# Kernel optimization log

Hardware: AMD Instinct MI355X
Metric: run time of the kernel (lower is better)

Reference implementation:

```python
import math
import jax, jax.numpy as jnp
import numpy as np

EPS = 1e-5

def lstm(x, Wih, Whh, b):
    # x: [N,T,D]; PyTorch gate order i,f,g,o; b = b_ih + b_hh combined
    N = x.shape[0]
    H = Whh.shape[1]
    gx = jnp.einsum('ntd,gd->ntg', x, Wih) + b  # [N,T,4H]
    def step(carry, g):
        h, c = carry
        z = g + h @ Whh.T
        i, f, gg, o = jnp.split(z, 4, axis=-1)
        c = jax.nn.sigmoid(f) * c + jax.nn.sigmoid(i) * jnp.tanh(gg)
        h = jax.nn.sigmoid(o) * jnp.tanh(c)
        return (h, c), h
    init = (jnp.zeros((N, H), x.dtype), jnp.zeros((N, H), x.dtype))
    (hN, _), ys = jax.lax.scan(step, init, jnp.swapaxes(gx, 0, 1))
    return jnp.swapaxes(ys, 0, 1), hN  # outputs [N,T,H], h_n [N,H]

def bilstm_layer(x, fW, fU, fb, bW, bU, bb):
    of, _ = lstm(x, fW, fU, fb)
    ob, _ = lstm(x[:, ::-1], bW, bU, bb)
    return jnp.concatenate([of, ob[:, ::-1]], axis=-1)

def layernorm(x, g, b):
    m = jnp.mean(x, -1, keepdims=True)
    v = jnp.mean((x - m) ** 2, -1, keepdims=True)
    return (x - m) * jax.lax.rsqrt(v + EPS) * g + b

def encoder_layer(src, Wq, bq, Wk, bk, Wv, bv, Wo, bo, W1, b1, W2, b2, lng, lnb):
    B, S, d = src.shape
    G, NH = 5, 5
    dk = d // NH
    # group channel shuffle (as in source)
    qs = src.reshape(B, S, G, d // G).swapaxes(-1, -2).reshape(B, S, d)
    q = qs @ Wq.T + bq
    k = q @ Wk.T + bk   # NOTE: source applies W_k/W_v to the projected query
    v = q @ Wv.T + bv
    def heads(t):
        return t.reshape(B, S, NH, dk).transpose(0, 2, 1, 3)
    qh, kh, vh = heads(q), heads(k), heads(v)
    attn = jax.nn.softmax(jnp.einsum('bhqd,bhkd->bhqk', qh, kh) / math.sqrt(dk), axis=-1)
    o = jnp.einsum('bhqk,bhkd->bhqd', attn, vh).transpose(0, 2, 1, 3).reshape(B, S, d)
    o = o @ Wo.T + bo
    src = layernorm(src + o, lng, lnb)          # dropout is identity in eval
    ff = jax.nn.relu(src @ W1.T + b1) @ W2.T + b2
    src = layernorm(src + ff, lng, lnb)         # same LayerNorm params reused
    return src, attn

def _forward(x, qWih, qWhh, qb, kWih, kWhh, kb, vWih, vWhh, vb,
             tWq, tbq, tWk, tbk, tWv, tbv, tWo, tbo, tW1, tb1, tW2, tb2, tlng, tlnb,
             l0fWih, l0fWhh, l0fb, l0bWih, l0bWhh, l0bb,
             l1fWih, l1fWhh, l1fb, l1bWih, l1bWhh, l1bb,
             fc1W, fc1b, fc2W, fc2b):
    B, T, F = x.shape
    H = qWhh.shape[1]
    # per-feature LSTMs: shared weights across features -> batch them
    xf = x.transpose(0, 2, 1).reshape(B * F, T, 1)
    _, hq = lstm(xf, qWih, qWhh, qb)   # [B*F,H]
    _, hk = lstm(xf, kWih, kWhh, kb)   # [B*F,H]
    _, hv = lstm(xf, vWih, vWhh, vb)   # [B*F,1]
    Q = hq.reshape(B, F, H)
    K = hk.reshape(B, F, H)
    V = hv.reshape(B, F)
    # b_ij = (q_i . k_j)/sqrt(H) * v_j, softmax over j
    scores = jnp.einsum('bih,bjh->bij', Q, K) / math.sqrt(H) * V[:, None, :]
    Wsm = jax.nn.softmax(scores, axis=-1)          # [B,F,F] rows indexed by i
    attn_output = jnp.einsum('btj,bij->bti', x, Wsm)  # bmm(x, softmax_b_i)
    b = Wsm.transpose(0, 2, 1)                     # stack(b_list, dim=-1)
    src = jnp.concatenate([x, attn_output], axis=-1)  # [B,T,2F]
    attns = []
    for l in range(2):
        src, a = encoder_layer(src, tWq[l], tbq[l], tWk[l], tbk[l], tWv[l], tbv[l],
                               tWo[l], tbo[l], tW1[l], tb1[l], tW2[l], tb2[l],
                               tlng[l], tlnb[l])
        attns.append(a)
    c = jnp.stack(attns)                           # [2,B,5,T,T]
    out = bilstm_layer(src, l0fWih, l0fWhh, l0fb, l0bWih, l0bWhh, l0bb)
    out = bilstm_layer(out, l1fWih, l1fWhh, l1fb, l1bWih, l1bWhh, l1bb)
    out = jax.nn.relu(out[:, -1, :])               # [B,2H]
    out = jax.nn.relu(out @ fc1W.T + fc1b)
    out = out @ fc2W.T + fc2b                      # [B,1]
    return out, b, c

def setup_inputs() -> dict:
    B, T, F, H = 16, 128, 40, 64
    d = 2 * F
    key = jax.random.key(0)
    ks = iter(jax.random.split(key, 64))
    def n(shape, fan):
        return (jax.random.normal(next(ks), shape) / math.sqrt(fan)).astype(jnp.float32)
    inp = {'x': jax.random.normal(next(ks), (B, T, F), dtype=jnp.float32)}
    # per-feature LSTMs
    inp.update(qWih=n((4 * H, 1), 1), qWhh=n((4 * H, H), H), qb=n((4 * H,), H))
    inp.update(kWih=n((4 * H, 1), 1), kWhh=n((4 * H, H), H), kb=n((4 * H,), H))
    inp.update(vWih=n((4, 1), 1), vWhh=n((4, 1), 1), vb=n((4,), 1))
    # transformer (2 layers stacked on leading axis)
    inp.update(tWq=n((2, d, d), d), tbq=n((2, d), d), tWk=n((2, d, d), d), tbk=n((2, d), d),
               tWv=n((2, d, d), d), tbv=n((2, d), d), tWo=n((2, d, d), d), tbo=n((2, d), d),
               tW1=n((2, 4 * d, d), d), tb1=n((2, 4 * d), d), tW2=n((2, d, 4 * d), 4 * d),
               tb2=n((2, d), 4 * d), tlng=jnp.ones((2, d), jnp.float32), tlnb=jnp.zeros((2, d), jnp.float32))
    # main bidirectional 2-layer LSTM
    inp.update(l0fWih=n((4 * H, d), d), l0fWhh=n((4 * H, H), H), l0fb=n((4 * H,), H),
               l0bWih=n((4 * H, d), d), l0bWhh=n((4 * H, H), H), l0bb=n((4 * H,), H),
               l1fWih=n((4 * H, 2 * H), 2 * H), l1fWhh=n((4 * H, H), H), l1fb=n((4 * H,), H),
               l1bWih=n((4 * H, 2 * H), 2 * H), l1bWhh=n((4 * H, H), H), l1bb=n((4 * H,), H))
    inp.update(fc1W=n((H, 2 * H), 2 * H), fc1b=n((H,), 2 * H), fc2W=n((1, H), H), fc2b=n((1,), H))
    return inp

def reference(x, qWih, qWhh, qb, kWih, kWhh, kb, vWih, vWhh, vb,
              tWq, tbq, tWk, tbk, tWv, tbv, tWo, tbo, tW1, tb1, tW2, tb2, tlng, tlnb,
              l0fWih, l0fWhh, l0fb, l0bWih, l0bWhh, l0bb,
              l1fWih, l1fWhh, l1fb, l1bWih, l1bWhh, l1bb,
              fc1W, fc1b, fc2W, fc2b):
    return _forward(x, qWih, qWhh, qb, kWih, kWhh, kb, vWih, vWhh, vb,
                    tWq, tbq, tWk, tbk, tWv, tbv, tWo, tbo, tW1, tb1, tW2, tb2, tlng, tlnb,
                    l0fWih, l0fWhh, l0fb, l0bWih, l0bWhh, l0bb,
                    l1fWih, l1fWhh, l1fb, l1bWih, l1bWhh, l1bb,
                    fc1W, fc1b, fc2W, fc2b)
```

## Files before the change

### kernel.cpp

```cpp
#include <hip/hip_runtime.h>

__device__ __forceinline__ float sigf(float x){ return 1.0f/(1.0f+__expf(-x)); }
__device__ __forceinline__ float tanhfast(float x){ return 1.0f - 2.0f/(__expf(2.0f*x)+1.0f); }

#define Bn 16
#define Tn 128
#define Fn 40
#define Hn 64
#define Dn 80
#define NHn 5
#define DKn 16
#define FFn 320

#define LD4(p,i) (((const float4*)(p))[i])

#define DECL16(v, p) \
  float4 v##0=LD4(p,0),  v##1=LD4(p,1),  v##2=LD4(p,2),  v##3=LD4(p,3),  \
         v##4=LD4(p,4),  v##5=LD4(p,5),  v##6=LD4(p,6),  v##7=LD4(p,7),  \
         v##8=LD4(p,8),  v##9=LD4(p,9),  v##10=LD4(p,10),v##11=LD4(p,11),\
         v##12=LD4(p,12),v##13=LD4(p,13),v##14=LD4(p,14),v##15=LD4(p,15);
#define PIN4(P) asm volatile("" : "+v"(P.x), "+v"(P.y), "+v"(P.z), "+v"(P.w));
#define PIN16(v) PIN4(v##0) PIN4(v##1) PIN4(v##2) PIN4(v##3) PIN4(v##4) PIN4(v##5) \
  PIN4(v##6) PIN4(v##7) PIN4(v##8) PIN4(v##9) PIN4(v##10) PIN4(v##11) PIN4(v##12) \
  PIN4(v##13) PIN4(v##14) PIN4(v##15)

#define ACC1(i) { const float4 hv = hb4[i]; \
  a += hv.x*w##i.x + hv.y*w##i.y + hv.z*w##i.z + hv.w*w##i.w; }
#define ACCROW ACC1(0) ACC1(1) ACC1(2) ACC1(3) ACC1(4) ACC1(5) ACC1(6) ACC1(7) \
  ACC1(8) ACC1(9) ACC1(10) ACC1(11) ACC1(12) ACC1(13) ACC1(14) ACC1(15)

__global__ __launch_bounds__(256) __attribute__((amdgpu_waves_per_eu(1,4)))
void k_feat_lstm4(
    const float* __restrict__ x,
    const float* __restrict__ qWih, const float* __restrict__ qWhh, const float* __restrict__ qb,
    const float* __restrict__ kWih, const float* __restrict__ kWhh, const float* __restrict__ kb,
    const float* __restrict__ vWih, const float* __restrict__ vWhh, const float* __restrict__ vb,
    float* __restrict__ hq, float* __restrict__ hk, float* __restrict__ hv)
{
  const int blk = blockIdx.x;
  const int t = threadIdx.x;
  if (blk >= 1280){
    const int inst = (blk - 1280)*256 + t;
    if (inst < 640){
      const int bi = inst/Fn, f = inst%Fn;
      const float* xp = x + bi*Tn*Fn + f;
      const float wih0=vWih[0], wih1=vWih[1], wih2=vWih[2], wih3=vWih[3];
      const float u0v=vWhh[0], u1v=vWhh[1], u2v=vWhh[2], u3v=vWhh[3];
      const float c0=vb[0], c1=vb[1], c2=vb[2], c3=vb[3];
      float h=0.f, c=0.f;
      #pragma unroll 1
      for (int tt=0;tt<Tn;++tt){
        float xt = xp[tt*Fn];
        float zi = xt*wih0 + h*u0v + c0;
        float zf = xt*wih1 + h*u1v + c1;
        float zg = xt*wih2 + h*u2v + c2;
        float zo = xt*wih3 + h*u3v + c3;
        c = sigf(zf)*c + sigf(zi)*tanhfast(zg);
        h = sigf(zo)*tanhfast(c);
      }
      hv[inst] = h;
    }
    return;
  }
  const bool isk = blk >= 640;
  const int inst = isk ? blk-640 : blk;
  const int bi = inst/Fn, f = inst%Fn;
  const float* Whh = isk ? kWhh : qWhh;
  const float* Wih = isk ? kWih : qWih;
  const float* bia = isk ? kb  : qb;
  float* outp = isk ? hk : hq;

  DECL16(w, Whh + t*Hn);
  PIN16(w);
  const float wih = Wih[t];
  const float bb  = bia[t];

  __shared__ __align__(16) float hb[Hn];
  __shared__ float zb[4*Hn];
  __shared__ float xls[Tn];

  const float* xp = x + bi*Tn*Fn + f;
  if (t < Tn) xls[t] = xp[t*Fn];
  if (t < Hn) hb[t] = 0.f;
  float c = 0.f, h = 0.f;
  __syncthreads();

  const float4* hb4 = (const float4*)hb;
  #pragma unroll 1
  for (int tt=0;tt<Tn;++tt){
    const float xt = xls[tt];
    float a = bb + xt*wih;
    ACCROW
    zb[t] = a;
    __syncthreads();
    if (t < Hn){
      const float zi = zb[t], zf = zb[t+64], zg = zb[t+128], zo = zb[t+192];
      c = sigf(zf)*c + sigf(zi)*tanhfast(zg);
      h = sigf(zo)*tanhfast(c);
      hb[t] = h;
    }
    __syncthreads();
  }
  if (t < Hn) outp[inst*Hn + t] = h;
}

__global__ __launch_bounds__(64) void k_featattn(
    const float* __restrict__ hq, const float* __restrict__ hk, const float* __restrict__ hv,
    float* __restrict__ Wsm, float* __restrict__ out_b)
{
  const int blk = blockIdx.x;
  const int bi = blk / Fn, i = blk % Fn;
  const int j = threadIdx.x;
  __shared__ float qrow[Hn];
  qrow[j] = hq[blk*Hn + j];
  __syncthreads();
  float s = -1e30f;
  if (j < Fn){
    const float* krow = hk + (bi*Fn + j)*Hn;
    float a = 0.f;
    #pragma unroll
    for (int h2=0; h2<Hn; ++h2) a += qrow[h2]*krow[h2];
    s = a * 0.125f * hv[bi*Fn + j];
  }
  float m = s;
  #pragma unroll
  for (int off=32; off>0; off>>=1) m = fmaxf(m, __shfl_xor(m, off));
  float e = (j < Fn) ? __expf(s - m) : 0.f;
  float tot = e;
  #pragma unroll
  for (int off=32; off>0; off>>=1) tot += __shfl_xor(tot, off);
  float p = e / tot;
  if (j < Fn){
    Wsm[blk*Fn + j] = p;
    out_b[bi*(Fn*Fn) + j*Fn + i] = p;
  }
}

__global__ __launch_bounds__(128) void k_build_src(
    const float* __restrict__ x, const float* __restrict__ Wsm, float* __restrict__ src)
{
  const int blk = blockIdx.x;
  const int bi = blk / Tn;
  const int tid = threadIdx.x;
  __shared__ float xrow[Fn];
  if (tid < Fn) xrow[tid] = x[blk*Fn + tid];
  __syncthreads();
  if (tid < Fn){
    src[blk*Dn + tid] = xrow[tid];
  } else if (tid < Dn){
    const int i = tid - Fn;
    const float* wrow = Wsm + (bi*Fn + i)*Fn;
    float a = 0.f;
    #pragma unroll
    for (int j2=0;j2<Fn;++j2) a += xrow[j2]*wrow[j2];
    src[blk*Dn + tid] = a;
  }
}

__global__ __launch_bounds__(128) void k_qkv(
    const float* __restrict__ src,
    const float* __restrict__ Wq, const float* __restrict__ bq,
    const float* __restrict__ Wk, const float* __restrict__ bk,
    const float* __restrict__ Wv, const float* __restrict__ bv,
    float* __restrict__ q, float* __restrict__ k, float* __restrict__ v)
{
  const int row = blockIdx.x;
  const int t = threadIdx.x;
  __shared__ float qs[Dn];
  __shared__ float qrow[Dn];
  if (t < Dn) qs[t] = src[row*Dn + (t%5)*16 + t/5];
  __syncthreads();
  if (t < Dn){
    const float* wr = Wq + t*Dn;
    float a = bq[t];
    #pragma unroll 8
    for (int d2=0; d2<Dn; ++d2) a += qs[d2]*wr[d2];
    qrow[t] = a;
    q[row*Dn + t] = a;
  }
  __syncthreads();
  if (t < Dn){
    const float* wk = Wk + t*Dn;
    const float* wv = Wv + t*Dn;
    float ak = bk[t], av = bv[t];
    #pragma unroll 8
    for (int d2=0; d2<Dn; ++d2){ float qq = qrow[d2]; ak += qq*wk[d2]; av += qq*wv[d2]; }
    k[row*Dn + t] = ak;
    v[row*Dn + t] = av;
  }
}

__global__ __launch_bounds__(128) void k_attn(
    const float* __restrict__ q, const float* __restrict__ k, const float* __restrict__ v,
    float* __restrict__ o, float* __restrict__ c_out)
{
  const int s1 = blockIdx.x, h = blockIdx.y, bi = blockIdx.z;
  const int s2 = threadIdx.x;
  __shared__ float qf[DKn];
  __shared__ float p[Tn];
  __shared__ float red_m[2];
  __shared__ float red_s[2];
  if (s2 < DKn) qf[s2] = q[(bi*Tn + s1)*Dn + h*DKn + s2];
  __syncthreads();
  const float* krow = k + (bi*Tn + s2)*Dn + h*DKn;
  float a = 0.f;
  #pragma unroll
  for (int d2=0; d2<DKn; ++d2) a += qf[d2]*krow[d2];
  a *= 0.25f;
  const int wv_id = s2 >> 6;
  float m = a;
  #pragma unroll
  for (int off=32; off>0; off>>=1) m = fmaxf(m, __shfl_xor(m, off));
  if ((s2 & 63) == 0) red_m[wv_id] = m;
  __syncthreads();
  m = fmaxf(red_m[0], red_m[1]);
  float e = __expf(a - m);
  float tot = e;
  #pragma unroll
  for (int off=32; off>0; off>>=1) tot += __shfl_xor(tot, off);
  if ((s2 & 63) == 0) red_s[wv_id] = tot;
  __syncthreads();
  tot = red_s[0] + red_s[1];
  float pv = e / tot;
  p[s2] = pv;
  c_out[((bi*NHn + h)*Tn + s1)*Tn + s2] = pv;
  __syncthreads();
  if (s2 < DKn){
    const float* vcol = v + bi*Tn*Dn + h*DKn + s2;
    float acc = 0.f;
    for (int j2=0;j2<Tn;++j2) acc += p[j2]*vcol[j2*Dn];
    o[(bi*Tn + s1)*Dn + h*DKn + s2] = acc;
  }
}

__global__ __launch_bounds__(320) void k_oln_ffln(
    const float* __restrict__ o, const float* __restrict__ Wo, const float* __restrict__ bo,
    const float* __restrict__ W1, const float* __restrict__ b1,
    const float* __restrict__ W2, const float* __restrict__ b2,
    const float* __restrict__ lng, const float* __restrict__ lnb, float* __restrict__ src)
{
  const int row = blockIdx.x;
  const int t = threadIdx.x;
  __shared__ float orow[Dn];
  __shared__ float s1row[Dn];
  __shared__ float h1[FFn];
  __shared__ float red[128];
  if (t < Dn) orow[t] = o[row*Dn + t];
  __syncthreads();
  float val = 0.f;
  if (t < Dn){
    const float* wr = Wo + t*Dn;
    float a = bo[t];
    #pragma unroll 8
    for (int d2=0; d2<Dn; ++d2) a += orow[d2]*wr[d2];
    val = a + src[row*Dn + t];
  }
  if (t < 128) red[t] = (t < Dn) ? val : 0.f;
  __syncthreads();
  for (int s=64; s>0; s>>=1){ if (t < s) red[t] += red[t+s]; __syncthreads(); }
  float mean = red[0] * (1.f/Dn);
  __syncthreads();
  if (t < 128){ float dv = (t < Dn) ? (val - mean) : 0.f; red[t] = dv*dv; }
  __syncthreads();
  for (int s=64; s>0; s>>=1){ if (t < s) red[t] += red[t+s]; __syncthreads(); }
  float rstd = rsqrtf(red[0]*(1.f/Dn) + 1e-5f);
  if (t < Dn) s1row[t] = (val - mean)*rstd*lng[t] + lnb[t];
  __syncthreads();
  {
    const float* wr = W1 + t*Dn;
    float a = b1[t];
    #pragma unroll 8
    for (int d2=0; d2<Dn; ++d2) a += s1row[d2]*wr[d2];
    h1[t] = fmaxf(a, 0.f);
  }
  __syncthreads();
  float val2 = 0.f;
  if (t < Dn){
    const float* wr = W2 + t*FFn;
    float a = b2[t];
    #pragma unroll 8
    for (int d2=0; d2<FFn; ++d2) a += h1[d2]*wr[d2];
    val2 = a + s1row[t];
  }
  if (t < 128) red[t] = (t < Dn) ? val2 : 0.f;
  __syncthreads();
  for (int s=64; s>0; s>>=1){ if (t < s) red[t] += red[t+s]; __syncthreads(); }
  mean = red[0] * (1.f/Dn);
  __syncthreads();
  if (t < 128){ float dv = (t < Dn) ? (val2 - mean) : 0.f; red[t] = dv*dv; }
  __syncthreads();
  for (int s=64; s>0; s>>=1){ if (t < s) red[t] += red[t+s]; __syncthreads(); }
  rstd = rsqrtf(red[0]*(1.f/Dn) + 1e-5f);
  if (t < Dn) src[row*Dn + t] = (val2 - mean)*rstd*lng[t] + lnb[t];
}

__global__ __launch_bounds__(256) void k_gx(
    const float* __restrict__ X, int inD,
    const float* __restrict__ WihF, const float* __restrict__ bF,
    const float* __restrict__ WihB, const float* __restrict__ bB,
    float* __restrict__ gx)
{
  const int row = blockIdx.x;
  const int dir = blockIdx.y;
  const int g = threadIdx.x;
  __shared__ float xs[128];
  for (int d2=g; d2<inD; d2+=256) xs[d2] = X[row*inD + d2];
  __syncthreads();
  const float* W  = dir ? WihB : WihF;
  const float* bb = dir ? bB  : bF;
  const float* wr = W + g*inD;
  float a = bb[g];
  for (int d2=0; d2<inD; ++d2) a += xs[d2]*wr[d2];
  gx[dir*(Bn*Tn*256) + row*256 + g] = a;
}

__global__ __launch_bounds__(256) __attribute__((amdgpu_waves_per_eu(1,4)))
void k_bilstm_rec4(
    const float* __restrict__ gx,
    const float* __restrict__ WhhF, const float* __restrict__ WhhB,
    float* __restrict__ outp)
{
  const int n = blockIdx.x;
  const int dir = blockIdx.y;
  const int t = threadIdx.x;
  const float* Whh = dir ? WhhB : WhhF;
  DECL16(w, Whh + t*Hn);
  PIN16(w);

  __shared__ __align__(16) float hb[Hn];
  __shared__ float zb[4*Hn];
  if (t < Hn) hb[t] = 0.f;
  float c = 0.f, h = 0.f;
  __syncthreads();

  const float* gxd = gx + dir*(Bn*Tn*256) + n*Tn*256;
  const float4* hb4 = (const float4*)hb;
  const int t0 = dir ? Tn-1 : 0;
  float g0 = gxd[t0*256 + t];
  #pragma unroll 1
  for (int step=0; step<Tn; ++step){
    const int tt = dir ? (Tn-1-step) : step;
    int tn = dir ? (Tn-2-step) : (step+1);
    tn = max(0, min(Tn-1, tn));
    const float p0 = gxd[tn*256 + t];
    float a = g0;
    ACCROW
    zb[t] = a;
    __syncthreads();
    if (t < Hn){
      const float zi = zb[t], zf = zb[t+64], zg = zb[t+128], zo = zb[t+192];
      c = sigf(zf)*c + sigf(zi)*tanhfast(zg);
      h = sigf(zo)*tanhfast(c);
      hb[t] = h;
      outp[(n*Tn + tt)*128 + dir*Hn + t] = h;
    }
    __syncthreads();
    g0 = p0;
  }
}

__global__ __launch_bounds__(128) void k_final(
    const float* __restrict__ out1,
    const float* __restrict__ fc1W, const float* __restrict__ fc1b,
    const float* __restrict__ fc2W, const float* __restrict__ fc2b,
    float* __restrict__ outp)
{
  const int n = blockIdx.x;
  const int t = threadIdx.x;
  __shared__ float r[128];
  __shared__ float a1[64];
  r[t] = fmaxf(out1[(n*Tn + (Tn-1))*128 + t], 0.f);
  __syncthreads();
  if (t < 64){
    const float* wr = fc1W + t*128;
    float a = fc1b[t];
    #pragma unroll 8
    for (int d2=0; d2<128; ++d2) a += r[d2]*wr[d2];
    a1[t] = fmaxf(a, 0.f);
  }
  __syncthreads();
  if (t == 0){
    float a = fc2b[0];
    #pragma unroll 8
    for (int d2=0; d2<64; ++d2) a += a1[d2]*fc2W[d2];
    outp[n] = a;
  }
}

extern "C" void kernel_launch(void* const* d_in, const int* in_sizes, int n_in,
                              void* d_out, int out_size, void* d_ws, size_t ws_size,
                              hipStream_t stream)
{
  const float* x     = (const float*)d_in[0];
  const float* qWih  = (const float*)d_in[1];
  const float* qWhh  = (const float*)d_in[2];
  const float* qb    = (const float*)d_in[3];
  const float* kWih  = (const float*)d_in[4];
  const float* kWhh  = (const float*)d_in[5];
  const float* kb    = (const float*)d_in[6];
  const float* vWih  = (const float*)d_in[7];
  const float* vWhh  = (const float*)d_in[8];
  const float* vb    = (const float*)d_in[9];
  const float* tWq   = (const float*)d_in[10];
  const float* tbq   = (const float*)d_in[11];
  const float* tWk   = (const float*)d_in[12];
  const float* tbk   = (const float*)d_in[13];
  const float* tWv   = (const float*)d_in[14];
  const float* tbv   = (const float*)d_in[15];
  const float* tWo   = (const float*)d_in[16];
  const float* tbo   = (const float*)d_in[17];
  const float* tW1   = (const float*)d_in[18];
  const float* tb1   = (const float*)d_in[19];
  const float* tW2   = (const float*)d_in[20];
  const float* tb2   = (const float*)d_in[21];
  const float* tlng  = (const float*)d_in[22];
  const float* tlnb  = (const float*)d_in[23];
  const float* l0fWih= (const float*)d_in[24];
  const float* l0fWhh= (const float*)d_in[25];
  const float* l0fb  = (const float*)d_in[26];
  const float* l0bWih= (const float*)d_in[27];
  const float* l0bWhh= (const float*)d_in[28];
  const float* l0bb  = (const float*)d_in[29];
  const float* l1fWih= (const float*)d_in[30];
  const float* l1fWhh= (const float*)d_in[31];
  const float* l1fb  = (const float*)d_in[32];
  const float* l1bWih= (const float*)d_in[33];
  const float* l1bWhh= (const float*)d_in[34];
  const float* l1bb  = (const float*)d_in[35];
  const float* fc1W  = (const float*)d_in[36];
  const float* fc1b  = (const float*)d_in[37];
  const float* fc2W  = (const float*)d_in[38];
  const float* fc2b  = (const float*)d_in[39];

  float* ws  = (float*)d_ws;
  float* hq  = ws;
  float* hk  = hq  + 640*64;
  float* hv  = hk  + 640*64;
  float* Wsm = hv  + 640;
  float* src = Wsm + 16*40*40;
  float* q   = src + 16*128*80;
  float* k   = q   + 16*128*80;
  float* v   = k   + 16*128*80;
  float* o   = v   + 16*128*80;
  float* gx  = o   + 16*128*80;
  float* lout0 = gx + 2*16*128*256;
  float* lout1 = lout0 + 16*128*128;

  float* outp  = (float*)d_out;
  float* out_b = outp + 16;
  float* out_c = out_b + 16*40*40;

  k_feat_lstm4<<<1283, 256, 0, stream>>>(x, qWih,qWhh,qb, kWih,kWhh,kb, vWih,vWhh,vb, hq,hk,hv);
  k_featattn<<<640, 64, 0, stream>>>(hq, hk, hv, Wsm, out_b);
  k_build_src<<<2048, 128, 0, stream>>>(x, Wsm, src);
  for (int l=0; l<2; ++l){
    k_qkv<<<2048, 128, 0, stream>>>(src, tWq + l*Dn*Dn, tbq + l*Dn,
                                    tWk + l*Dn*Dn, tbk + l*Dn,
                                    tWv + l*Dn*Dn, tbv + l*Dn, q, k, v);
    k_attn<<<dim3(128,5,16), 128, 0, stream>>>(q, k, v, o, out_c + (size_t)l*16*5*128*128);
    k_oln_ffln<<<2048, 320, 0, stream>>>(o, tWo + l*Dn*Dn, tbo + l*Dn,
                                         tW1 + l*FFn*Dn, tb1 + l*FFn,
                                         tW2 + l*Dn*FFn, tb2 + l*Dn,
                                         tlng + l*Dn, tlnb + l*Dn, src);
  }
  k_gx<<<dim3(2048,2), 256, 0, stream>>>(src, 80, l0fWih, l0fb, l0bWih, l0bb, gx);
  k_bilstm_rec4<<<dim3(16,2), 256, 0, stream>>>(gx, l0fWhh, l0bWhh, lout0);
  k_gx<<<dim3(2048,2), 256, 0, stream>>>(lout0, 128, l1fWih, l1fb, l1bWih, l1bb, gx);
  k_bilstm_rec4<<<dim3(16,2), 256, 0, stream>>>(gx, l1fWhh, l1bWhh, lout1);
  k_final<<<16, 128, 0, stream>>>(lout1, fc1W, fc1b, fc2W, fc2b, outp);
}
```

Before: 814.5 us.

## Split LSTM recurrent matvec across 4 lanes per gate row with shuffle reduction

The recurrent LSTM kernels (feature LSTMs and the bidirectional main LSTM) now use 1024-thread blocks. Each gate row's 64-wide dot product with h is split across 4 lanes of 16 elements each, and the partial sums are combined with xor shuffles. This shortens the serial per-step matvec latency on the critical recurrent chain and cuts weight registers per thread. The cost is larger blocks, more expensive __syncthreads across 16 waves, and extra shuffle steps each timestep.

```diff
diff --git a/kernel.cpp b/kernel.cpp
--- a/kernel.cpp
+++ b/kernel.cpp
@@ -13,24 +13,19 @@
 #define FFn 320
 
 #define LD4(p,i) (((const float4*)(p))[i])
-
-#define DECL16(v, p) \
-  float4 v##0=LD4(p,0),  v##1=LD4(p,1),  v##2=LD4(p,2),  v##3=LD4(p,3),  \
-         v##4=LD4(p,4),  v##5=LD4(p,5),  v##6=LD4(p,6),  v##7=LD4(p,7),  \
-         v##8=LD4(p,8),  v##9=LD4(p,9),  v##10=LD4(p,10),v##11=LD4(p,11),\
-         v##12=LD4(p,12),v##13=LD4(p,13),v##14=LD4(p,14),v##15=LD4(p,15);
+#define DECL4(v, p) \
+  float4 v##0=LD4(p,0), v##1=LD4(p,1), v##2=LD4(p,2), v##3=LD4(p,3);
 #define PIN4(P) asm volatile("" : "+v"(P.x), "+v"(P.y), "+v"(P.z), "+v"(P.w));
-#define PIN16(v) PIN4(v##0) PIN4(v##1) PIN4(v##2) PIN4(v##3) PIN4(v##4) PIN4(v##5) \
-  PIN4(v##6) PIN4(v##7) PIN4(v##8) PIN4(v##9) PIN4(v##10) PIN4(v##11) PIN4(v##12) \
-  PIN4(v##13) PIN4(v##14) PIN4(v##15)
-
-#define ACC1(i) { const float4 hv = hb4[i]; \
-  a += hv.x*w##i.x + hv.y*w##i.y + hv.z*w##i.z + hv.w*w##i.w; }
-#define ACCROW ACC1(0) ACC1(1) ACC1(2) ACC1(3) ACC1(4) ACC1(5) ACC1(6) ACC1(7) \
-  ACC1(8) ACC1(9) ACC1(10) ACC1(11) ACC1(12) ACC1(13) ACC1(14) ACC1(15)
-
-__global__ __launch_bounds__(256) __attribute__((amdgpu_waves_per_eu(1,4)))
-void k_feat_lstm4(
+#define PINW(v) PIN4(v##0) PIN4(v##1) PIN4(v##2) PIN4(v##3)
+
+#define DOT16(jc4) \
+  { const float4 h0=hb4[(jc4)+0]; a += h0.x*w0.x + h0.y*w0.y + h0.z*w0.z + h0.w*w0.w; } \
+  { const float4 h1=hb4[(jc4)+1]; a += h1.x*w1.x + h1.y*w1.y + h1.z*w1.z + h1.w*w1.w; } \
+  { const float4 h2=hb4[(jc4)+2]; a += h2.x*w2.x + h2.y*w2.y + h2.z*w2.z + h2.w*w2.w; } \
+  { const float4 h3=hb4[(jc4)+3]; a += h3.x*w3.x + h3.y*w3.y + h3.z*w3.z + h3.w*w3.w; }
+
+__global__ __launch_bounds__(1024)
+void k_feat_lstm6(
     const float* __restrict__ x,
     const float* __restrict__ qWih, const float* __restrict__ qWhh, const float* __restrict__ qb,
     const float* __restrict__ kWih, const float* __restrict__ kWhh, const float* __restrict__ kb,
@@ -40,7 +35,7 @@
   const int blk = blockIdx.x;
   const int t = threadIdx.x;
   if (blk >= 1280){
-    const int inst = (blk - 1280)*256 + t;
+    const int inst = t;
     if (inst < 640){
       const int bi = inst/Fn, f = inst%Fn;
       const float* xp = x + bi*Tn*Fn + f;
@@ -70,34 +65,42 @@
   const float* bia = isk ? kb  : qb;
   float* outp = isk ? hk : hq;
 
-  DECL16(w, Whh + t*Hn);
-  PIN16(w);
-  const float wih = Wih[t];
-  const float bb  = bia[t];
-
-  __shared__ __align__(16) float hb[Hn];
-  __shared__ float zb[4*Hn];
+  const int lane = t & 63;
+  const int wv   = t >> 6;
+  const int r16  = lane & 15;
+  const int jc   = lane >> 4;
+  const int row  = wv*16 + r16;
+  const int jc4  = jc*4;
+
+  DECL4(w, Whh + row*Hn + jc*16);
+  PINW(w);
+  const float wih = Wih[row];
+  const float bb  = bia[row];
+
+  __shared__ __align__(16) float hls[Hn];
+  __shared__ float zls[4*Hn];
   __shared__ float xls[Tn];
 
   const float* xp = x + bi*Tn*Fn + f;
   if (t < Tn) xls[t] = xp[t*Fn];
-  if (t < Hn) hb[t] = 0.f;
+  if (t < Hn) hls[t] = 0.f;
   float c = 0.f, h = 0.f;
   __syncthreads();
 
-  const float4* hb4 = (const float4*)hb;
+  const float4* hb4 = (const float4*)hls;
   #pragma unroll 1
   for (int tt=0;tt<Tn;++tt){
-    const float xt = xls[tt];
-    float a = bb + xt*wih;
-    ACCROW
-    zb[t] = a;
+    float a = (jc==0) ? (bb + xls[tt]*wih) : 0.f;
+    DOT16(jc4)
+    a += __shfl_xor(a, 16);
+    a += __shfl_xor(a, 32);
+    if (jc==0) zls[row] = a;
     __syncthreads();
     if (t < Hn){
-      const float zi = zb[t], zf = zb[t+64], zg = zb[t+128], zo = zb[t+192];
+      const float zi = zls[t], zf = zls[t+64], zg = zls[t+128], zo = zls[t+192];
       c = sigf(zf)*c + sigf(zi)*tanhfast(zg);
       h = sigf(zo)*tanhfast(c);
-      hb[t] = h;
+      hls[t] = h;
     }
     __syncthreads();
   }
@@ -314,8 +317,8 @@
   gx[dir*(Bn*Tn*256) + row*256 + g] = a;
 }
 
-__global__ __launch_bounds__(256) __attribute__((amdgpu_waves_per_eu(1,4)))
-void k_bilstm_rec4(
+__global__ __launch_bounds__(1024)
+void k_bilstm_rec6(
     const float* __restrict__ gx,
     const float* __restrict__ WhhF, const float* __restrict__ WhhB,
     float* __restrict__ outp)
@@ -323,35 +326,43 @@
   const int n = blockIdx.x;
   const int dir = blockIdx.y;
   const int t = threadIdx.x;
+  const int lane = t & 63;
+  const int wv   = t >> 6;
+  const int r16  = lane & 15;
+  const int jc   = lane >> 4;
+  const int row  = wv*16 + r16;
+  const int jc4  = jc*4;
   const float* Whh = dir ? WhhB : WhhF;
-  DECL16(w, Whh + t*Hn);
-  PIN16(w);
-
-  __shared__ __align__(16) float hb[Hn];
-  __shared__ float zb[4*Hn];
-  if (t < Hn) hb[t] = 0.f;
+  DECL4(w, Whh + row*Hn + jc*16);
+  PINW(w);
+
+  __shared__ __align__(16) float hls[Hn];
+  __shared__ float zls[4*Hn];
+  if (t < Hn) hls[t] = 0.f;
   float c = 0.f, h = 0.f;
   __syncthreads();
 
   const float* gxd = gx + dir*(Bn*Tn*256) + n*Tn*256;
-  const float4* hb4 = (const float4*)hb;
+  const float4* hb4 = (const float4*)hls;
   const int t0 = dir ? Tn-1 : 0;
-  float g0 = gxd[t0*256 + t];
+  float g0 = (jc==0) ? gxd[t0*256 + row] : 0.f;
   #pragma unroll 1
   for (int step=0; step<Tn; ++step){
     const int tt = dir ? (Tn-1-step) : step;
     int tn = dir ? (Tn-2-step) : (step+1);
     tn = max(0, min(Tn-1, tn));
-    const float p0 = gxd[tn*256 + t];
+    const float p0 = (jc==0) ? gxd[tn*256 + row] : 0.f;
     float a = g0;
-    ACCROW
-    zb[t] = a;
+    DOT16(jc4)
+    a += __shfl_xor(a, 16);
+    a += __shfl_xor(a, 32);
+    if (jc==0) zls[row] = a;
     __syncthreads();
     if (t < Hn){
-      const float zi = zb[t], zf = zb[t+64], zg = zb[t+128], zo = zb[t+192];
+      const float zi = zls[t], zf = zls[t+64], zg = zls[t+128], zo = zls[t+192];
       c = sigf(zf)*c + sigf(zi)*tanhfast(zg);
       h = sigf(zo)*tanhfast(c);
-      hb[t] = h;
+      hls[t] = h;
       outp[(n*Tn + tt)*128 + dir*Hn + t] = h;
     }
     __syncthreads();
@@ -450,7 +461,7 @@
   float* out_b = outp + 16;
   float* out_c = out_b + 16*40*40;
 
-  k_feat_lstm4<<<1283, 256, 0, stream>>>(x, qWih,qWhh,qb, kWih,kWhh,kb, vWih,vWhh,vb, hq,hk,hv);
+  k_feat_lstm6<<<1281, 1024, 0, stream>>>(x, qWih,qWhh,qb, kWih,kWhh,kb, vWih,vWhh,vb, hq,hk,hv);
   k_featattn<<<640, 64, 0, stream>>>(hq, hk, hv, Wsm, out_b);
   k_build_src<<<2048, 128, 0, stream>>>(x, Wsm, src);
   for (int l=0; l<2; ++l){
@@ -464,8 +475,8 @@
                                          tlng + l*Dn, tlnb + l*Dn, src);
   }
   k_gx<<<dim3(2048,2), 256, 0, stream>>>(src, 80, l0fWih, l0fb, l0bWih, l0bb, gx);
-  k_bilstm_rec4<<<dim3(16,2), 256, 0, stream>>>(gx, l0fWhh, l0bWhh, lout0);
+  k_bilstm_rec6<<<dim3(16,2), 1024, 0, stream>>>(gx, l0fWhh, l0bWhh, lout0);
   k_gx<<<dim3(2048,2), 256, 0, stream>>>(lout0, 128, l1fWih, l1fb, l1bWih, l1bb, gx);
-  k_bilstm_rec4<<<dim3(16,2), 256, 0, stream>>>(gx, l1fWhh, l1bWhh, lout1);
+  k_bilstm_rec6<<<dim3(16,2), 1024, 0, stream>>>(gx, l1fWhh, l1bWhh, lout1);
   k_final<<<16, 128, 0, stream>>>(lout1, fc1W, fc1b, fc2W, fc2b, outp);
 }
```

Result: slower. 890.0 us (+9.3%).
